# Kernel optimization log

Hardware: AMD Instinct MI355X
Metric: run time of the kernel (lower is better)

## Reference

```python
import jax, jax.numpy as jnp
import numpy as np

M, N, C, D = 2, 8, 1024, 256  # n_routers, num_adapters, channel_dim, down_sample_size
B, S = 32, 512


def setup_inputs() -> dict:
    key = jax.random.key(0)
    k1, k2, k3, k4, k5 = jax.random.split(key, 5)
    x = jax.random.normal(k1, (B, S, C), dtype=jnp.float32)
    expert_index = jax.random.randint(k2, (M, B), 0, N, dtype=jnp.int32)
    down_w = jax.random.normal(k3, (M, N, C, D), dtype=jnp.float32) * 0.01
    down_b = jax.random.normal(k4, (M, N, D), dtype=jnp.float32) * 0.01
    up_w = jax.random.normal(k5, (M, N, D, C), dtype=jnp.float32) * 0.01
    return {"x": x, "expert_index": expert_index, "down_w": down_w,
            "down_b": down_b, "up_w": up_w}


def reference(x, expert_index, down_w, down_b, up_w):
    # Gather per-(router, batch-element) adapter weights along the adapter axis.
    idx = expert_index  # [M, B]
    bw_down = jnp.take_along_axis(down_w, idx[:, :, None, None], axis=1)  # [M, B, C, D]
    bb_down = jnp.take_along_axis(down_b, idx[:, :, None], axis=1)        # [M, B, D]
    bw_up = jnp.take_along_axis(up_w, idx[:, :, None, None], axis=1)      # [M, B, D, C]
    # z = swish(x @ W_down + b_down)  -> [M, B, S, D]
    z = jnp.einsum('bsc,mbcd->mbsd', x, bw_down) + bb_down[:, :, None, :]
    z = jax.nn.silu(z)
    # u = z @ W_up -> [M, B, S, C]
    u = jnp.einsum('mbsd,mbdc->mbsc', z, bw_up)
    return u
```

## Files before the change

### kernel.cpp

```cpp
#include <hip/hip_runtime.h>
#include <stdint.h>

typedef unsigned short u16;
typedef __bf16 bf16x8 __attribute__((ext_vector_type(8)));
typedef float f32x4 __attribute__((ext_vector_type(4)));

#define MM 2
#define NN 8
#define CC 1024
#define DD 256
#define BB 32
#define SS 512

__device__ __forceinline__ u16 f2bf(float f) {
  uint32_t u = __float_as_uint(f);
  u += 0x7FFFu + ((u >> 16) & 1u);
  return (u16)(u >> 16);
}

__device__ __forceinline__ uint32_t pack2(float a, float b) {
  return (uint32_t)f2bf(a) | ((uint32_t)f2bf(b) << 16);
}

__device__ __forceinline__ void async16(const void* g, void* l) {
  __builtin_amdgcn_global_load_lds(
      (const __attribute__((address_space(1))) uint32_t*)g,
      (__attribute__((address_space(3))) uint32_t*)l, 16, 0, 0);
}

__global__ __launch_bounds__(256) void prep_w(
    const float* __restrict__ dw, u16* __restrict__ wdT,
    const float* __restrict__ uw, u16* __restrict__ wuT) {
  __shared__ float tile[64][33];
  int bid = blockIdx.x;
  const float* src; u16* dst; int K, N, tk, tn;
  if (bid < 2048) {
    K = CC; N = DD;
    const int slab = bid >> 7, t = bid & 127;
    tk = t >> 3; tn = t & 7;
    src = dw + (size_t)slab * K * N;
    dst = wdT + (size_t)slab * K * N;
  } else {
    bid -= 2048;
    K = DD; N = CC;
    const int slab = bid >> 7, t = bid & 127;
    tk = t >> 5; tn = t & 31;
    src = uw + (size_t)slab * K * N;
    dst = wuT + (size_t)slab * K * N;
  }
  const int k0 = tk * 64, n0 = tn * 32;
  const int tx = threadIdx.x & 31, ty = threadIdx.x >> 5;
#pragma unroll
  for (int i = 0; i < 64; i += 8)
    tile[ty + i][tx] = src[(size_t)(k0 + ty + i) * N + n0 + tx];
  __syncthreads();
  uint32_t* dst32 = reinterpret_cast<uint32_t*>(dst);
#pragma unroll
  for (int i = 0; i < 32; i += 8) {
    const int nr = ty + i;
    dst32[((size_t)(n0 + nr) * K + k0) / 2 + tx] =
        pack2(tile[2 * tx][nr], tile[2 * tx + 1][nr]);
  }
}

__global__ __launch_bounds__(512, 2) void fused_adapter(
    const float* __restrict__ x, const u16* __restrict__ wdT,
    const u16* __restrict__ wuT, const float* __restrict__ db,
    const int* __restrict__ eidx, float* __restrict__ out) {
  __shared__ __align__(16) u16 smA[2][128 * 64];
  __shared__ __align__(16) u16 smB[2][256 * 64];
  __shared__ __align__(16) u16 zl[8 * 128 * 32];

  const int pair = blockIdx.y;
  const int m = pair >> 5;
  const int b = pair & 31;
  const int e = eidx[pair];
  const int s0 = blockIdx.x * 128;

  const int tid = threadIdx.x;
  const int lane = tid & 63;
  const int wave = tid >> 6;
  const int quad = lane >> 4;
  const int l16 = lane & 15;
  const int fx = (l16 >> 1) & 3;
  const int fxr = l16 & 7;

  const int wr = (wave >> 2) * 64;
  const int wc = (wave & 3) * 64;

  const u16* Bd = wdT + (size_t)(m * NN + e) * DD * CC;
  const u16* Bu = wuT + (size_t)(m * NN + e) * CC * DD;

  const float* bias_p = db + (size_t)(m * NN + e) * DD;
  float biasr[4];
#pragma unroll
  for (int j = 0; j < 4; ++j) biasr[j] = bias_p[wc + j * 16 + l16];

  const int arow = tid >> 2;
  const int c0 = tid & 3;
  const float* gAx = x + ((size_t)b * SS + s0 + arow) * CC;
  const int lA0 = arow * 64 + ((c0 ^ (arow & 7)) * 8);
  const int lA1 = arow * 64 + (((c0 + 4) ^ (arow & 7)) * 8);

  const int r_l = lane >> 3;
  const int sx = (lane & 7) ^ r_l;

  f32x4 acc[4][4];
#pragma unroll
  for (int i = 0; i < 4; ++i)
#pragma unroll
    for (int j = 0; j < 4; ++j) acc[i][j] = (f32x4){0.f, 0.f, 0.f, 0.f};

  {
    float4 a0 = *reinterpret_cast<const float4*>(gAx + c0 * 8);
    float4 a1 = *reinterpret_cast<const float4*>(gAx + c0 * 8 + 4);
    float4 a2 = *reinterpret_cast<const float4*>(gAx + (c0 + 4) * 8);
    float4 a3 = *reinterpret_cast<const float4*>(gAx + (c0 + 4) * 8 + 4);
#pragma unroll
    for (int s = 0; s < 4; ++s)
      async16(Bd + (size_t)(wave * 32 + s * 8 + r_l) * CC + sx * 8,
              &smB[0][(wave * 32 + s * 8) * 64]);
    *reinterpret_cast<uint4*>(&smA[0][lA0]) =
        make_uint4(pack2(a0.x, a0.y), pack2(a0.z, a0.w),
                   pack2(a1.x, a1.y), pack2(a1.z, a1.w));
    *reinterpret_cast<uint4*>(&smA[0][lA1]) =
        make_uint4(pack2(a2.x, a2.y), pack2(a2.z, a2.w),
                   pack2(a3.x, a3.y), pack2(a3.z, a3.w));
  }
  asm volatile("s_waitcnt vmcnt(0) lgkmcnt(0)" ::: "memory");
  __builtin_amdgcn_s_barrier();

  for (int kk = 0; kk < 16; ++kk) {
    const int cur = kk & 1, nxt = cur ^ 1;
    float4 a0, a1, a2, a3;
    if (kk < 15) {
      const float* gA = gAx + (kk + 1) * 64;
      a0 = *reinterpret_cast<const float4*>(gA + c0 * 8);
      a1 = *reinterpret_cast<const float4*>(gA + c0 * 8 + 4);
      a2 = *reinterpret_cast<const float4*>(gA + (c0 + 4) * 8);
      a3 = *reinterpret_cast<const float4*>(gA + (c0 + 4) * 8 + 4);
      const int ko = (kk + 1) * 64;
#pragma unroll
      for (int s = 0; s < 4; ++s)
        async16(Bd + (size_t)(wave * 32 + s * 8 + r_l) * CC + ko + sx * 8,
                &smB[nxt][(wave * 32 + s * 8) * 64]);
    } else {
#pragma unroll
      for (int s = 0; s < 4; ++s)
        async16(Bu + (size_t)(wave * 32 + s * 8 + r_l) * DD + sx * 8,
                &smB[nxt][(wave * 32 + s * 8) * 64]);
    }
#pragma unroll
    for (int h = 0; h < 2; ++h) {
      bf16x8 af[4], bfr[4];
#pragma unroll
      for (int i = 0; i < 4; ++i)
        af[i] = *reinterpret_cast<const bf16x8*>(
            &smA[cur][(wr + i * 16 + l16) * 64 + ((h * 4 + quad) ^ fxr) * 8]);
#pragma unroll
      for (int j = 0; j < 4; ++j)
        bfr[j] = *reinterpret_cast<const bf16x8*>(
            &smB[cur][(wc + j * 16 + l16) * 64 + ((h * 4 + quad) ^ fxr) * 8]);
      __builtin_amdgcn_s_setprio(1);
#pragma unroll
      for (int i = 0; i < 4; ++i)
#pragma unroll
        for (int j = 0; j < 4; ++j)
          acc[i][j] = __builtin_amdgcn_mfma_f32_16x16x32_bf16(af[i], bfr[j], acc[i][j], 0, 0, 0);
      __builtin_amdgcn_s_setprio(0);
    }
    if (kk < 15) {
      *reinterpret_cast<uint4*>(&smA[nxt][lA0]) =
          make_uint4(pack2(a0.x, a0.y), pack2(a0.z, a0.w),
                     pack2(a1.x, a1.y), pack2(a1.z, a1.w));
      *reinterpret_cast<uint4*>(&smA[nxt][lA1]) =
          make_uint4(pack2(a2.x, a2.y), pack2(a2.z, a2.w),
                     pack2(a3.x, a3.y), pack2(a3.z, a3.w));
    }
    asm volatile("s_waitcnt vmcnt(0) lgkmcnt(0)" ::: "memory");
    __builtin_amdgcn_s_barrier();
  }

#pragma unroll
  for (int j = 0; j < 4; ++j) {
    const int d = wc + j * 16 + l16;
    const int kt = d >> 5;
    const int kl = d & 31;
    const int slot0 = kl >> 3;
    const int kin = kl & 7;
#pragma unroll
    for (int i = 0; i < 4; ++i) {
      const int zr = wr + i * 16 + quad * 4;
#pragma unroll
      for (int r = 0; r < 4; ++r) {
        const int row = zr + r;
        float v = acc[i][j][r] + biasr[j];
        v = v / (1.f + __expf(-v));
        zl[kt * 4096 + row * 32 + ((slot0 ^ ((row >> 1) & 3)) * 8) + kin] = f2bf(v);
      }
    }
  }
  asm volatile("s_waitcnt lgkmcnt(0)" ::: "memory");
  __builtin_amdgcn_s_barrier();

  float* ob = out + ((size_t)pair * SS + s0) * CC;

  for (int g = 0; g < 16; ++g) {
    const int cur2 = g & 1, nxt2 = cur2 ^ 1;
    const int ct = g >> 2;
    const int it2 = g & 3;
    if (g < 15) {
      const int g2 = g + 1;
      const size_t ro = (size_t)(g2 >> 2) * 256 * DD + (g2 & 3) * 64;
#pragma unroll
      for (int s = 0; s < 4; ++s)
        async16(Bu + ro + (size_t)(wave * 32 + s * 8 + r_l) * DD + sx * 8,
                &smB[nxt2][(wave * 32 + s * 8) * 64]);
    }
    if (it2 == 0) {
#pragma unroll
      for (int i = 0; i < 4; ++i)
#pragma unroll
        for (int j = 0; j < 4; ++j) acc[i][j] = (f32x4){0.f, 0.f, 0.f, 0.f};
    }
#pragma unroll
    for (int h = 0; h < 2; ++h) {
      bf16x8 af[4], bfr[4];
#pragma unroll
      for (int i = 0; i < 4; ++i)
        af[i] = *reinterpret_cast<const bf16x8*>(
            &zl[(it2 * 2 + h) * 4096 + (wr + i * 16 + l16) * 32 + (quad ^ fx) * 8]);
#pragma unroll
      for (int j = 0; j < 4; ++j)
        bfr[j] = *reinterpret_cast<const bf16x8*>(
            &smB[cur2][(wc + j * 16 + l16) * 64 + ((h * 4 + quad) ^ fxr) * 8]);
      __builtin_amdgcn_s_setprio(1);
#pragma unroll
      for (int i = 0; i < 4; ++i)
#pragma unroll
        for (int j = 0; j < 4; ++j)
          acc[i][j] = __builtin_amdgcn_mfma_f32_16x16x32_bf16(af[i], bfr[j], acc[i][j], 0, 0, 0);
      __builtin_amdgcn_s_setprio(0);
    }
    if (it2 == 3) {
#pragma unroll
      for (int j = 0; j < 4; ++j) {
        const int c = ct * 256 + wc + j * 16 + l16;
#pragma unroll
        for (int i = 0; i < 4; ++i) {
          const int sr = wr + i * 16 + quad * 4;
#pragma unroll
          for (int r = 0; r < 4; ++r)
            ob[(size_t)(sr + r) * CC + c] = acc[i][j][r];
        }
      }
    }
    if (g < 15) {
      asm volatile("s_waitcnt vmcnt(0) lgkmcnt(0)" ::: "memory");
      __builtin_amdgcn_s_barrier();
    }
  }
}

extern "C" void kernel_launch(void* const* d_in, const int* in_sizes, int n_in,
                              void* d_out, int out_size, void* d_ws, size_t ws_size,
                              hipStream_t stream) {
  const float* x  = (const float*)d_in[0];
  const int* eidx = (const int*)d_in[1];
  const float* dw = (const float*)d_in[2];
  const float* db = (const float*)d_in[3];
  const float* uw = (const float*)d_in[4];
  float* out = (float*)d_out;

  char* ws = (char*)d_ws;
  u16* wdT = (u16*)(ws);
  u16* wuT = (u16*)(ws + (size_t)8 * 1024 * 1024);

  prep_w<<<dim3(4096), dim3(256), 0, stream>>>(dw, wdT, uw, wuT);
  fused_adapter<<<dim3(SS / 128, MM * BB), dim3(512), 0, stream>>>(
      x, wdT, wuT, db, eidx, out);
}
```

Baseline: 247.3 us.

## Pre-convert x to bf16 and load A tiles via async LDS copies with XCD-aware block mapping

Adds a pass to the prep kernel that converts x from fp32 to bf16 in workspace. The fused kernel then streams A tiles into LDS with global_load_lds, the same way as the weights, instead of loading fp32 into registers, packing and writing to LDS. It also flattens the grid to 1D and remaps block ids so each XCD handles a fixed group of batch elements, both routers and all s-tiles, for better L2 reuse of x. The cost is an extra full pass over x (read fp32, write bf16) and larger workspace use, in exchange for halving A-tile bytes in the main loop and removing register pressure and conversion work there.

```diff
diff --git a/kernel.cpp b/kernel.cpp
--- a/kernel.cpp
+++ b/kernel.cpp
@@ -30,9 +30,22 @@
 
 __global__ __launch_bounds__(256) void prep_w(
     const float* __restrict__ dw, u16* __restrict__ wdT,
-    const float* __restrict__ uw, u16* __restrict__ wuT) {
+    const float* __restrict__ uw, u16* __restrict__ wuT,
+    const float* __restrict__ x, u16* __restrict__ xb) {
+  int bid = blockIdx.x;
+  if (bid >= 4096) {
+    const int t = bid - 4096;
+    const float4* in4 = reinterpret_cast<const float4*>(x) + (size_t)t * 2048;
+    uint2* out2 = reinterpret_cast<uint2*>(xb) + (size_t)t * 2048;
+    const int tx = threadIdx.x;
+#pragma unroll
+    for (int k = 0; k < 8; ++k) {
+      float4 v = in4[k * 256 + tx];
+      out2[k * 256 + tx] = make_uint2(pack2(v.x, v.y), pack2(v.z, v.w));
+    }
+    return;
+  }
   __shared__ float tile[64][33];
-  int bid = blockIdx.x;
   const float* src; u16* dst; int K, N, tk, tn;
   if (bid < 2048) {
     K = CC; N = DD;
@@ -64,18 +77,22 @@
 }
 
 __global__ __launch_bounds__(512, 2) void fused_adapter(
-    const float* __restrict__ x, const u16* __restrict__ wdT,
+    const u16* __restrict__ xb, const u16* __restrict__ wdT,
     const u16* __restrict__ wuT, const float* __restrict__ db,
     const int* __restrict__ eidx, float* __restrict__ out) {
   __shared__ __align__(16) u16 smA[2][128 * 64];
   __shared__ __align__(16) u16 smB[2][256 * 64];
   __shared__ __align__(16) u16 zl[8 * 128 * 32];
 
-  const int pair = blockIdx.y;
-  const int m = pair >> 5;
-  const int b = pair & 31;
+  const int id = blockIdx.x;
+  const int xcd = id & 7;
+  const int j5 = id >> 3;
+  const int stile = j5 >> 3;
+  const int m = (j5 >> 2) & 1;
+  const int b = xcd * 4 + (j5 & 3);
+  const int pair = m * BB + b;
   const int e = eidx[pair];
-  const int s0 = blockIdx.x * 128;
+  const int s0 = stile * 128;
 
   const int tid = threadIdx.x;
   const int lane = tid & 63;
@@ -96,59 +113,42 @@
 #pragma unroll
   for (int j = 0; j < 4; ++j) biasr[j] = bias_p[wc + j * 16 + l16];
 
-  const int arow = tid >> 2;
-  const int c0 = tid & 3;
-  const float* gAx = x + ((size_t)b * SS + s0 + arow) * CC;
-  const int lA0 = arow * 64 + ((c0 ^ (arow & 7)) * 8);
-  const int lA1 = arow * 64 + (((c0 + 4) ^ (arow & 7)) * 8);
-
   const int r_l = lane >> 3;
   const int sx = (lane & 7) ^ r_l;
 
+  const u16* gA = xb + ((size_t)b * SS + s0 + wave * 16 + r_l) * CC + sx * 8;
+  const u16* gBd = Bd + (size_t)(wave * 32 + r_l) * CC + sx * 8;
+  const u16* gBu = Bu + (size_t)(wave * 32 + r_l) * DD + sx * 8;
+
   f32x4 acc[4][4];
 #pragma unroll
   for (int i = 0; i < 4; ++i)
 #pragma unroll
     for (int j = 0; j < 4; ++j) acc[i][j] = (f32x4){0.f, 0.f, 0.f, 0.f};
 
-  {
-    float4 a0 = *reinterpret_cast<const float4*>(gAx + c0 * 8);
-    float4 a1 = *reinterpret_cast<const float4*>(gAx + c0 * 8 + 4);
-    float4 a2 = *reinterpret_cast<const float4*>(gAx + (c0 + 4) * 8);
-    float4 a3 = *reinterpret_cast<const float4*>(gAx + (c0 + 4) * 8 + 4);
-#pragma unroll
-    for (int s = 0; s < 4; ++s)
-      async16(Bd + (size_t)(wave * 32 + s * 8 + r_l) * CC + sx * 8,
-              &smB[0][(wave * 32 + s * 8) * 64]);
-    *reinterpret_cast<uint4*>(&smA[0][lA0]) =
-        make_uint4(pack2(a0.x, a0.y), pack2(a0.z, a0.w),
-                   pack2(a1.x, a1.y), pack2(a1.z, a1.w));
-    *reinterpret_cast<uint4*>(&smA[0][lA1]) =
-        make_uint4(pack2(a2.x, a2.y), pack2(a2.z, a2.w),
-                   pack2(a3.x, a3.y), pack2(a3.z, a3.w));
-  }
+#pragma unroll
+  for (int s = 0; s < 2; ++s)
+    async16(gA + (size_t)(s * 8) * CC, &smA[0][(wave * 16 + s * 8) * 64]);
+#pragma unroll
+  for (int s = 0; s < 4; ++s)
+    async16(gBd + (size_t)(s * 8) * CC, &smB[0][(wave * 32 + s * 8) * 64]);
   asm volatile("s_waitcnt vmcnt(0) lgkmcnt(0)" ::: "memory");
   __builtin_amdgcn_s_barrier();
 
   for (int kk = 0; kk < 16; ++kk) {
     const int cur = kk & 1, nxt = cur ^ 1;
-    float4 a0, a1, a2, a3;
     if (kk < 15) {
-      const float* gA = gAx + (kk + 1) * 64;
-      a0 = *reinterpret_cast<const float4*>(gA + c0 * 8);
-      a1 = *reinterpret_cast<const float4*>(gA + c0 * 8 + 4);
-      a2 = *reinterpret_cast<const float4*>(gA + (c0 + 4) * 8);
-      a3 = *reinterpret_cast<const float4*>(gA + (c0 + 4) * 8 + 4);
       const int ko = (kk + 1) * 64;
 #pragma unroll
+      for (int s = 0; s < 2; ++s)
+        async16(gA + (size_t)(s * 8) * CC + ko, &smA[nxt][(wave * 16 + s * 8) * 64]);
+#pragma unroll
       for (int s = 0; s < 4; ++s)
-        async16(Bd + (size_t)(wave * 32 + s * 8 + r_l) * CC + ko + sx * 8,
-                &smB[nxt][(wave * 32 + s * 8) * 64]);
+        async16(gBd + (size_t)(s * 8) * CC + ko, &smB[nxt][(wave * 32 + s * 8) * 64]);
     } else {
 #pragma unroll
       for (int s = 0; s < 4; ++s)
-        async16(Bu + (size_t)(wave * 32 + s * 8 + r_l) * DD + sx * 8,
-                &smB[nxt][(wave * 32 + s * 8) * 64]);
+        async16(gBu + (size_t)(s * 8) * DD, &smB[nxt][(wave * 32 + s * 8) * 64]);
     }
 #pragma unroll
     for (int h = 0; h < 2; ++h) {
@@ -168,14 +168,6 @@
         for (int j = 0; j < 4; ++j)
           acc[i][j] = __builtin_amdgcn_mfma_f32_16x16x32_bf16(af[i], bfr[j], acc[i][j], 0, 0, 0);
       __builtin_amdgcn_s_setprio(0);
-    }
-    if (kk < 15) {
-      *reinterpret_cast<uint4*>(&smA[nxt][lA0]) =
-          make_uint4(pack2(a0.x, a0.y), pack2(a0.z, a0.w),
-                     pack2(a1.x, a1.y), pack2(a1.z, a1.w));
-      *reinterpret_cast<uint4*>(&smA[nxt][lA1]) =
-          make_uint4(pack2(a2.x, a2.y), pack2(a2.z, a2.w),
-                     pack2(a3.x, a3.y), pack2(a3.z, a3.w));
     }
     asm volatile("s_waitcnt vmcnt(0) lgkmcnt(0)" ::: "memory");
     __builtin_amdgcn_s_barrier();
@@ -214,8 +206,7 @@
       const size_t ro = (size_t)(g2 >> 2) * 256 * DD + (g2 & 3) * 64;
 #pragma unroll
       for (int s = 0; s < 4; ++s)
-        async16(Bu + ro + (size_t)(wave * 32 + s * 8 + r_l) * DD + sx * 8,
-                &smB[nxt2][(wave * 32 + s * 8) * 64]);
+        async16(gBu + ro + (size_t)(s * 8) * DD, &smB[nxt2][(wave * 32 + s * 8) * 64]);
     }
     if (it2 == 0) {
 #pragma unroll
@@ -275,8 +266,9 @@
   char* ws = (char*)d_ws;
   u16* wdT = (u16*)(ws);
   u16* wuT = (u16*)(ws + (size_t)8 * 1024 * 1024);
-
-  prep_w<<<dim3(4096), dim3(256), 0, stream>>>(dw, wdT, uw, wuT);
-  fused_adapter<<<dim3(SS / 128, MM * BB), dim3(512), 0, stream>>>(
-      x, wdT, wuT, db, eidx, out);
-}
+  u16* xbf = (u16*)(ws + (size_t)16 * 1024 * 1024);
+
+  prep_w<<<dim3(6144), dim3(256), 0, stream>>>(dw, wdT, uw, wuT, x, xbf);
+  fused_adapter<<<dim3(256), dim3(512), 0, stream>>>(
+      xbf, wdT, wuT, db, eidx, out);
+}
```

Measured after the change: 275.8 us. 1.12x slower.
